# Optimization experiments

Hardware: AMD Instinct MI355X
Metric: run time of the kernel (lower is better)

The kernel has to match this reference:

```python
import jax, jax.numpy as jnp
import numpy as np

K = 7          # kernel_size (square)
P = K // 2     # padding
NUM_HEADS = 12


def setup_inputs() -> dict:
    key = jax.random.key(0)
    ks = jax.random.split(key, 6)
    B, H, W, D = 16, 56, 56, 768
    x = jax.random.normal(ks[0], (B, H, W, D), jnp.float32)
    qkv_w = jax.random.normal(ks[1], (3 * D, D), jnp.float32) * 0.02
    qkv_b = jnp.zeros((3 * D,), jnp.float32)
    rel_bias = jax.random.normal(ks[2], (1, NUM_HEADS, 1, K * K), jnp.float32)
    proj_w = jax.random.normal(ks[3], (D, D), jnp.float32) * 0.02
    proj_b = jnp.zeros((D,), jnp.float32)
    return {"x": x, "qkv_w": qkv_w, "qkv_b": qkv_b, "rel_bias": rel_bias,
            "proj_w": proj_w, "proj_b": proj_b}


def reference(x, qkv_w, qkv_b, rel_bias, proj_w, proj_b):
    B, H, W, D = x.shape
    hd = D // NUM_HEADS
    scale = 1.0 / np.sqrt(hd)

    qkv = x @ qkv_w.T + qkv_b                       # [B,H,W,3D]
    qkv = jnp.pad(qkv, ((0, 0), (P, P), (P, P), (0, 0)))  # zero-pad spatially
    Hp, Wp = H + 2 * P, W + 2 * P
    qkv = qkv.reshape(B, Hp, Wp, 3, NUM_HEADS, hd)
    qkv = jnp.transpose(qkv, (3, 0, 4, 1, 2, 5))    # [3,B,nh,Hp,Wp,hd]
    qf, kf, vf = qkv[0], qkv[1], qkv[2]

    q = qf[:, :, P:P + H, P:P + W, :]               # [B,nh,H,W,hd] (center pixel queries)

    # validity of each padded position (out-of-bounds keys get -inf, matching the torch mask)
    valid = jnp.pad(jnp.ones((H, W), dtype=bool), ((P, P), (P, P)))

    # scores per kernel offset; offsets iterate row-major (di, dj) matching
    # torch.meshgrid(..., indexing='ij') flattening used for relative_position_bias
    scores = []
    for di in range(K):
        for dj in range(K):
            ksh = kf[:, :, di:di + H, dj:dj + W, :]           # shifted keys [B,nh,H,W,hd]
            s = jnp.einsum('bnhwd,bnhwd->bnhw', q, ksh) * scale
            s = s + rel_bias[0, :, 0, di * K + dj][None, :, None, None]
            vmask = valid[di:di + H, dj:dj + W]
            s = jnp.where(vmask[None, None, :, :], s, -jnp.inf)
            scores.append(s)
    scores = jnp.stack(scores, axis=-1)             # [B,nh,H,W,K*K]
    attn = jax.nn.softmax(scores, axis=-1)

    out = jnp.zeros_like(q)
    for di in range(K):
        for dj in range(K):
            vsh = vf[:, :, di:di + H, dj:dj + W, :]
            out = out + attn[..., di * K + dj, None] * vsh

    out = jnp.transpose(out, (0, 2, 3, 1, 4)).reshape(B, H, W, D)
    return out @ proj_w.T + proj_b
```

## Files before the change

### kernel.cpp

```cpp
#include <hip/hip_runtime.h>
#include <hip/hip_bf16.h>

typedef __attribute__((ext_vector_type(8))) short short8;
typedef __attribute__((ext_vector_type(4))) short s16x4;
typedef __attribute__((ext_vector_type(4))) float f32x4;

#define AS1 __attribute__((address_space(1)))
#define AS3 __attribute__((address_space(3)))

__device__ __forceinline__ void gld16(const short* g, short* l) {
  __builtin_amdgcn_global_load_lds((const AS1 void*)g, (AS3 void*)l, 16, 0, 0);
}

__device__ __forceinline__ float bf2f(short x) {
  return __uint_as_float(((unsigned)(unsigned short)x) << 16);
}
__device__ __forceinline__ short f2bf(float f) {
  unsigned u = __float_as_uint(f);
  return (short)((u + 0x7fffu + ((u >> 16) & 1u)) >> 16);
}
__device__ __forceinline__ short f2bfn(float f) {
  __hip_bfloat16 h = __float2bfloat16(f);
  return *reinterpret_cast<short*>(&h);
}

__global__ void cast_f32_bf16(const float* __restrict__ src, short* __restrict__ dst, int n8) {
  int stride = gridDim.x * blockDim.x;
  for (int i = blockIdx.x * blockDim.x + threadIdx.x; i < n8; i += stride) {
    const float4* s = (const float4*)(src + (size_t)i * 8);
    float4 a = s[0], b = s[1];
    short8 o;
    o[0] = f2bf(a.x); o[1] = f2bf(a.y); o[2] = f2bf(a.z); o[3] = f2bf(a.w);
    o[4] = f2bf(b.x); o[5] = f2bf(b.y); o[6] = f2bf(b.z); o[7] = f2bf(b.w);
    *(short8*)(dst + (size_t)i * 8) = o;
  }
}

template<int OUT_BF16>
__global__ __launch_bounds__(256, 2) void gemm_bt(
    const short* __restrict__ A, const short* __restrict__ Bm,
    const float* __restrict__ bias, void* __restrict__ C,
    int M, int N, int Kd, int NB)
{
  __shared__ short As[128 * 64];
  __shared__ short Bs[128 * 64];
  const int tid = threadIdx.x;
  const int wave = tid >> 6, lane = tid & 63;

  int nwg = gridDim.x;
  int chunk = nwg >> 3;
  int bid = blockIdx.x;
  int nb2 = (bid & 7) * chunk + (bid >> 3);
  int per = NB << 3;
  int sr = nb2 / per, rem = nb2 - sr * per;
  int nblk = rem >> 3, mrow = rem & 7;
  int mblk = sr * 8 + mrow;

  size_t arow0 = (size_t)mblk * 128;
  size_t brow0 = (size_t)nblk * 128;
  const int wm = wave >> 1, wn = wave & 1;
  const int lr = lane & 15, grp = lane >> 4;

  const short* gsa[4]; const short* gsb[4];
  short* lda[4]; short* ldb[4];
  #pragma unroll
  for (int i = 0; i < 4; ++i) {
    int f = i * 256 + wave * 64 + lane;
    int row = f >> 3;
    int colc = (f & 7) ^ (row & 7);
    gsa[i] = A  + (arow0 + row) * Kd + colc * 8;
    gsb[i] = Bm + (brow0 + row) * Kd + colc * 8;
    lda[i] = &As[(i * 256 + wave * 64) * 8];
    ldb[i] = &Bs[(i * 256 + wave * 64) * 8];
  }

  f32x4 acc[4][4];
  #pragma unroll
  for (int i = 0; i < 4; ++i)
    #pragma unroll
    for (int j = 0; j < 4; ++j) {
      acc[i][j][0] = 0.f; acc[i][j][1] = 0.f; acc[i][j][2] = 0.f; acc[i][j][3] = 0.f;
    }

  int aoff[4][2], boff[4][2];
  #pragma unroll
  for (int mi = 0; mi < 4; ++mi) {
    int arow = wm * 64 + mi * 16 + lr;
    int brow = wn * 64 + mi * 16 + lr;
    #pragma unroll
    for (int kk = 0; kk < 2; ++kk) {
      int cb = (kk * 64 + grp * 16);
      aoff[mi][kk] = arow * 64 + ((cb ^ ((arow & 7) << 4)) >> 1);
      boff[mi][kk] = brow * 64 + ((cb ^ ((brow & 7) << 4)) >> 1);
    }
  }

  for (int k0 = 0; k0 < Kd; k0 += 64) {
    #pragma unroll
    for (int i = 0; i < 4; ++i) {
      gld16(gsa[i] + k0, lda[i]);
      gld16(gsb[i] + k0, ldb[i]);
    }
    __syncthreads();
    short8 af[4][2], bfr[4][2];
    #pragma unroll
    for (int mi = 0; mi < 4; ++mi)
      #pragma unroll
      for (int kk = 0; kk < 2; ++kk) {
        af[mi][kk]  = *(const short8*)&As[aoff[mi][kk]];
        bfr[mi][kk] = *(const short8*)&Bs[boff[mi][kk]];
      }
    #pragma unroll
    for (int kk = 0; kk < 2; ++kk)
      #pragma unroll
      for (int i = 0; i < 4; ++i)
        #pragma unroll
        for (int j = 0; j < 4; ++j)
          acc[i][j] = __builtin_amdgcn_mfma_f32_16x16x32_bf16(af[i][kk], bfr[j][kk], acc[i][j], 0, 0, 0);
    __syncthreads();
  }

  int r0 = grp * 4;
  #pragma unroll
  for (int i = 0; i < 4; ++i) {
    size_t grow0 = arow0 + wm * 64 + i * 16 + r0;
    #pragma unroll
    for (int j = 0; j < 4; ++j) {
      size_t gcol = brow0 + wn * 64 + j * 16 + lr;
      float bv = bias[gcol];
      #pragma unroll
      for (int r = 0; r < 4; ++r) {
        float v = acc[i][j][r] + bv;
        size_t off = (grow0 + r) * (size_t)N + gcol;
        if (OUT_BF16) ((short*)C)[off] = f2bf(v);
        else          ((float*)C)[off] = v;
      }
    }
  }
}

__global__ void build_idx(unsigned char* __restrict__ idxt) {
  int tile = blockIdx.x;
  int ht = tile >> 2, wt = tile & 3;
  int tid = threadIdx.x;
  int wave = tid >> 6, lane = tid & 63;
  int grp = lane >> 4, q = lane & 15;
  int Sw = (22 * wave) & ~7;
  unsigned w[12];
  #pragma unroll
  for (int i = 0; i < 12; ++i) w[i] = 0x31313131u;
  #pragma unroll
  for (int kt = 0; kt < 10; ++kt) {
    unsigned wd = 0;
    #pragma unroll
    for (int r = 0; r < 4; ++r) {
      int i22 = Sw + kt * 16 + grp * 4 + r;
      int hr = i22 / 22, hc = i22 - hr * 22;
      int dr = hr - wave, dc = hc - q;
      int kh = ht * 4 - 3 + hr, kw = wt * 16 - 3 + hc;
      bool valid = ((unsigned)dr < 7u) && ((unsigned)dc < 7u) &&
                   ((unsigned)kh < 56u) && ((unsigned)kw < 56u);
      unsigned o = valid ? (unsigned)(dr * 7 + dc) : 49u;
      wd |= o << (r * 8);
    }
    w[kt] = wd;
  }
  uint4* dst = (uint4*)(idxt + (((size_t)tile * 4 + wave) * 64 + lane) * 48);
  dst[0] = make_uint4(w[0], w[1], w[2], w[3]);
  dst[1] = make_uint4(w[4], w[5], w[6], w[7]);
  dst[2] = make_uint4(w[8], w[9], w[10], w[11]);
}

#define HALO_V 232

__global__ __launch_bounds__(256, 4) void attn_mfma(
    const short* __restrict__ qkv, const float* __restrict__ rel_bias,
    const unsigned char* __restrict__ idxt, const short* __restrict__ zp,
    short* __restrict__ attn_out)
{
  __shared__ __align__(16) short kvbuf[HALO_V * 64];
  __shared__ float sbias[52];

  const int tid = threadIdx.x;
  const int wave = tid >> 6, lane = tid & 63;
  const int tile = blockIdx.x;
  const int ht = tile >> 2, wt = tile & 3;
  const int head = blockIdx.y % 12, b = blockIdx.y / 12;
  const int r0 = ht * 4, c0 = wt * 16;
  const int grp = lane >> 4, q = lane & 15;
  const int grp4 = grp * 4, grp8 = grp * 8;
  const int Sw = (22 * wave) & ~7;

  if (tid < 50) sbias[tid] = (tid < 49) ? rel_bias[head * 49 + tid] : -1e30f;

  const uint4* ip = (const uint4*)(idxt + (((size_t)tile * 4 + wave) * 64 + lane) * 48);
  uint4 iw0 = ip[0], iw1 = ip[1], iw2 = ip[2];
  unsigned idxw[10] = {iw0.x, iw0.y, iw0.z, iw0.w, iw1.x, iw1.y, iw1.z, iw1.w,
                       iw2.x, iw2.y};

  const int qrow = r0 + wave;
  const int qcol = min(c0 + q, 55);
  const short* qp = qkv + ((size_t)((b * 56 + qrow) * 56 + qcol)) * 2304 + head * 64;
  short8 qf0 = *(const short8*)(qp + grp8);
  short8 qf1 = *(const short8*)(qp + 32 + grp8);

  #pragma unroll
  for (int it = 0; it < 8; ++it) {
    int f = it * 256 + tid;
    if (f < HALO_V * 8) {
      int row = f >> 3, cc = f & 7;
      int hr = row / 22, hc = row - hr * 22;
      int gh = r0 - 3 + hr, gw = c0 - 3 + hc;
      bool ok = (row < 220) && ((unsigned)gh < 56u) && ((unsigned)gw < 56u);
      const short* src = ok
        ? qkv + ((size_t)((b * 56 + gh) * 56 + gw)) * 2304 + 768 + head * 64
              + ((cc ^ (row & 7)) * 8)
        : zp;
      gld16(src, &kvbuf[(it * 256 + wave * 64) * 8]);
    }
  }

  __syncthreads();

  short8 va[4], vb[4];
  int vq = 0, dcc = 0;
  const bool vact = (tid < HALO_V);
  if (vact) {
    vq = tid % 58; dcc = tid / 58;
    #pragma unroll
    for (int rr = 0; rr < 4; ++rr) {
      int vec = vq * 4 + rr;
      int hr = vec / 22, hc = vec - hr * 22;
      int gh = r0 - 3 + hr, gw = c0 - 3 + hc;
      bool ok = (vec < 220) && ((unsigned)gh < 56u) && ((unsigned)gw < 56u);
      const short8* vp = ok
        ? (const short8*)(qkv + ((size_t)((b * 56 + gh) * 56 + gw)) * 2304
                          + 1536 + head * 64 + dcc * 16)
        : (const short8*)zp;
      va[rr] = vp[0]; vb[rr] = vp[1];
    }
  }

  f32x4 accs[10];
  #pragma unroll
  for (int kt = 0; kt < 10; ++kt) {
    accs[kt][0] = 0.f; accs[kt][1] = 0.f; accs[kt][2] = 0.f; accs[kt][3] = 0.f;
  }
  #pragma unroll
  for (int kt = 0; kt < 10; ++kt) {
    int vec = Sw + kt * 16 + q;
    int sw = vec & 7;
    short8 k0 = *(const short8*)&kvbuf[vec * 64 + ((grp ^ sw)) * 8];
    short8 k1 = *(const short8*)&kvbuf[vec * 64 + (((grp + 4) ^ sw)) * 8];
    accs[kt] = __builtin_amdgcn_mfma_f32_16x16x32_bf16(k0, qf0, accs[kt], 0, 0, 0);
    accs[kt] = __builtin_amdgcn_mfma_f32_16x16x32_bf16(k1, qf1, accs[kt], 0, 0, 0);
  }

  __syncthreads();

  float mx = -1e30f;
  #pragma unroll
  for (int kt = 0; kt < 10; ++kt) {
    #pragma unroll
    for (int r = 0; r < 4; ++r) {
      float bia = sbias[(idxw[kt] >> (r * 8)) & 0xffu];
      float s = fmaf(accs[kt][r], 0.125f, bia);
      accs[kt][r] = s;
      mx = fmaxf(mx, s);
    }
  }
  mx = fmaxf(mx, __shfl_xor(mx, 16));
  mx = fmaxf(mx, __shfl_xor(mx, 32));
  float sum = 0.f;
  #pragma unroll
  for (int kt = 0; kt < 10; ++kt)
    #pragma unroll
    for (int r = 0; r < 4; ++r) {
      float e = __expf(accs[kt][r] - mx);
      accs[kt][r] = e;
      sum += e;
    }
  sum += __shfl_xor(sum, 16);
  sum += __shfl_xor(sum, 32);
  float inv = 1.0f / sum;

  if (vact) {
    #pragma unroll
    for (int dd = 0; dd < 8; ++dd) {
      s16x4 w;
      w[0] = va[0][dd]; w[1] = va[1][dd]; w[2] = va[2][dd]; w[3] = va[3][dd];
      *(s16x4*)&kvbuf[(dcc * 16 + dd) * HALO_V + vq * 4] = w;
    }
    #pragma unroll
    for (int dd = 0; dd < 8; ++dd) {
      s16x4 w;
      w[0] = vb[0][dd]; w[1] = vb[1][dd]; w[2] = vb[2][dd]; w[3] = vb[3][dd];
      *(s16x4*)&kvbuf[(dcc * 16 + 8 + dd) * HALO_V + vq * 4] = w;
    }
  }

  unsigned plo[10], phi[10];
  #pragma unroll
  for (int kt = 0; kt < 10; ++kt) {
    plo[kt] = (unsigned)(unsigned short)f2bfn(accs[kt][0])
            | ((unsigned)(unsigned short)f2bfn(accs[kt][1]) << 16);
    phi[kt] = (unsigned)(unsigned short)f2bfn(accs[kt][2])
            | ((unsigned)(unsigned short)f2bfn(accs[kt][3]) << 16);
  }

  __syncthreads();

  const int src0 = ((grp & 1) << 5) + q;
  const bool hi = (grp >> 1) & 1;
  f32x4 acco[4];
  #pragma unroll
  for (int dt = 0; dt < 4; ++dt) {
    acco[dt][0] = 0.f; acco[dt][1] = 0.f; acco[dt][2] = 0.f; acco[dt][3] = 0.f;
  }
  #pragma unroll
  for (int km = 0; km < 5; ++km) {
    int aw0 = __shfl((int)plo[2*km], src0),      bw0 = __shfl((int)plo[2*km+1], src0);
    int aw1 = __shfl((int)phi[2*km], src0),      bw1 = __shfl((int)phi[2*km+1], src0);
    int aw2 = __shfl((int)plo[2*km], src0 + 16), bw2 = __shfl((int)plo[2*km+1], src0 + 16);
    int aw3 = __shfl((int)phi[2*km], src0 + 16), bw3 = __shfl((int)phi[2*km+1], src0 + 16);
    int4 wv = make_int4(hi ? bw0 : aw0, hi ? bw1 : aw1,
                        hi ? bw2 : aw2, hi ? bw3 : aw3);
    short8 pf = *(short8*)&wv;
    #pragma unroll
    for (int dt = 0; dt < 4; ++dt) {
      short8 vf = *(const short8*)&kvbuf[(dt * 16 + q) * HALO_V + Sw + km * 32 + grp8];
      acco[dt] = __builtin_amdgcn_mfma_f32_16x16x32_bf16(pf, vf, acco[dt], 0, 0, 0);
    }
  }

  float invr[4];
  #pragma unroll
  for (int r = 0; r < 4; ++r) invr[r] = __shfl(inv, grp4 + r);
  #pragma unroll
  for (int dt = 0; dt < 4; ++dt) {
    #pragma unroll
    for (int r = 0; r < 4; ++r) {
      int qc = c0 + grp4 + r;
      if (qc < 56) {
        size_t off = ((size_t)((b * 56 + qrow) * 56 + qc)) * 768
                     + head * 64 + dt * 16 + q;
        attn_out[off] = f2bfn(acco[dt][r] * invr[r]);
      }
    }
  }
}

extern "C" void kernel_launch(void* const* d_in, const int* in_sizes, int n_in,
                              void* d_out, int out_size, void* d_ws, size_t ws_size,
                              hipStream_t stream)
{
  const float* x      = (const float*)d_in[0];
  const float* qkv_w  = (const float*)d_in[1];
  const float* qkv_b  = (const float*)d_in[2];
  const float* rel_b  = (const float*)d_in[3];
  const float* proj_w = (const float*)d_in[4];
  const float* proj_b = (const float*)d_in[5];

  char* ws = (char*)d_ws;
  short* x_bf    = (short*)(ws);
  short* attn_bf = (short*)(ws);
  short* qw_bf   = (short*)(ws + 77070336);
  short* pw_bf   = (short*)(ws + 80609280);
  short* qkv_bf  = (short*)(ws + 81788928);
  unsigned char* idxt = (unsigned char*)(ws + 312999936);
  short* zp      = (short*)(ws + 313688064);

  hipMemsetAsync(zp, 0, 256, stream);
  build_idx<<<56, 256, 0, stream>>>(idxt);

  cast_f32_bf16<<<2048, 256, 0, stream>>>(x, x_bf, 38535168 / 8);
  cast_f32_bf16<<<864, 256, 0, stream>>>(qkv_w, qw_bf, 1769472 / 8);
  cast_f32_bf16<<<288, 256, 0, stream>>>(proj_w, pw_bf, 589824 / 8);

  gemm_bt<1><<<392 * 18, 256, 0, stream>>>(x_bf, qw_bf, qkv_b, (void*)qkv_bf,
                                           50176, 2304, 768, 18);

  attn_mfma<<<dim3(56, 192), 256, 0, stream>>>(qkv_bf, rel_b, idxt, zp, attn_bf);

  gemm_bt<0><<<392 * 6, 256, 0, stream>>>(attn_bf, pw_bf, proj_b, d_out,
                                          50176, 768, 768, 6);
}
```

Measured before the change: 461.3 us.

## Use 256x256 double-buffered GEMM tiles with 512 threads and prefetch overlap

Replaces the 128x128 single-buffered bf16 GEMM with a 256x256 tile kernel run by 8 waves. Shared-memory loads are double-buffered so the next K-slice is fetched while MFMAs run, with explicit vmcnt waits, raw barriers and s_setprio around the MFMA blocks. The XCD-aware block remap is generalised to grid sizes not divisible by 8. The larger tile raises per-block reuse, but it uses 128KB of LDS and many accumulator registers, which can cut occupancy. The proj GEMM also drops to only 588 blocks, which may leave some compute units underused.

```diff
diff --git a/kernel.cpp b/kernel.cpp
--- a/kernel.cpp
+++ b/kernel.cpp
@@ -37,93 +37,123 @@
 }
 
 template<int OUT_BF16>
-__global__ __launch_bounds__(256, 2) void gemm_bt(
+__global__ __launch_bounds__(512, 2) void gemm256(
     const short* __restrict__ A, const short* __restrict__ Bm,
     const float* __restrict__ bias, void* __restrict__ C,
     int M, int N, int Kd, int NB)
 {
-  __shared__ short As[128 * 64];
-  __shared__ short Bs[128 * 64];
+  __shared__ short As[2][256 * 64];
+  __shared__ short Bs[2][256 * 64];
   const int tid = threadIdx.x;
   const int wave = tid >> 6, lane = tid & 63;
 
   int nwg = gridDim.x;
-  int chunk = nwg >> 3;
-  int bid = blockIdx.x;
-  int nb2 = (bid & 7) * chunk + (bid >> 3);
-  int per = NB << 3;
+  int q8 = nwg >> 3, r8 = nwg & 7;
+  int xcd = blockIdx.x & 7, loc = blockIdx.x >> 3;
+  int nb2 = (xcd < r8 ? xcd * (q8 + 1) : r8 * (q8 + 1) + (xcd - r8) * q8) + loc;
+  int per = NB << 2;
   int sr = nb2 / per, rem = nb2 - sr * per;
-  int nblk = rem >> 3, mrow = rem & 7;
-  int mblk = sr * 8 + mrow;
-
-  size_t arow0 = (size_t)mblk * 128;
-  size_t brow0 = (size_t)nblk * 128;
-  const int wm = wave >> 1, wn = wave & 1;
+  int nblk = rem >> 2, mrow = rem & 3;
+  int mblk = sr * 4 + mrow;
+
+  size_t arow0 = (size_t)mblk * 256;
+  size_t brow0 = (size_t)nblk * 256;
+  const int wm = wave >> 2, wn = wave & 3;
   const int lr = lane & 15, grp = lane >> 4;
 
-  const short* gsa[4]; const short* gsb[4];
-  short* lda[4]; short* ldb[4];
+  const short* gsa[4]; const short* gsb[4]; int sdst[4];
   #pragma unroll
   for (int i = 0; i < 4; ++i) {
-    int f = i * 256 + wave * 64 + lane;
+    int f = i * 512 + tid;
     int row = f >> 3;
     int colc = (f & 7) ^ (row & 7);
     gsa[i] = A  + (arow0 + row) * Kd + colc * 8;
     gsb[i] = Bm + (brow0 + row) * Kd + colc * 8;
-    lda[i] = &As[(i * 256 + wave * 64) * 8];
-    ldb[i] = &Bs[(i * 256 + wave * 64) * 8];
-  }
-
-  f32x4 acc[4][4];
-  #pragma unroll
-  for (int i = 0; i < 4; ++i)
+    sdst[i] = (i * 512 + wave * 64) * 8;
+  }
+
+  f32x4 acc[8][4];
+  #pragma unroll
+  for (int i = 0; i < 8; ++i)
     #pragma unroll
     for (int j = 0; j < 4; ++j) {
       acc[i][j][0] = 0.f; acc[i][j][1] = 0.f; acc[i][j][2] = 0.f; acc[i][j][3] = 0.f;
     }
 
-  int aoff[4][2], boff[4][2];
-  #pragma unroll
-  for (int mi = 0; mi < 4; ++mi) {
-    int arow = wm * 64 + mi * 16 + lr;
-    int brow = wn * 64 + mi * 16 + lr;
+  int aoff[8][2], boff[4][2];
+  #pragma unroll
+  for (int mi = 0; mi < 8; ++mi) {
+    int arow = wm * 128 + mi * 16 + lr;
     #pragma unroll
     for (int kk = 0; kk < 2; ++kk) {
-      int cb = (kk * 64 + grp * 16);
+      int cb = kk * 64 + grp * 16;
       aoff[mi][kk] = arow * 64 + ((cb ^ ((arow & 7) << 4)) >> 1);
-      boff[mi][kk] = brow * 64 + ((cb ^ ((brow & 7) << 4)) >> 1);
-    }
-  }
-
-  for (int k0 = 0; k0 < Kd; k0 += 64) {
-    #pragma unroll
-    for (int i = 0; i < 4; ++i) {
-      gld16(gsa[i] + k0, lda[i]);
-      gld16(gsb[i] + k0, ldb[i]);
-    }
-    __syncthreads();
-    short8 af[4][2], bfr[4][2];
-    #pragma unroll
-    for (int mi = 0; mi < 4; ++mi)
+    }
+  }
+  #pragma unroll
+  for (int nj = 0; nj < 4; ++nj) {
+    int brow = wn * 64 + nj * 16 + lr;
+    #pragma unroll
+    for (int kk = 0; kk < 2; ++kk) {
+      int cb = kk * 64 + grp * 16;
+      boff[nj][kk] = brow * 64 + ((cb ^ ((brow & 7) << 4)) >> 1);
+    }
+  }
+
+  const int NK = Kd >> 6;
+
+  #pragma unroll
+  for (int i = 0; i < 4; ++i) gld16(gsa[i], &As[0][sdst[i]]);
+  #pragma unroll
+  for (int i = 0; i < 4; ++i) gld16(gsb[i], &Bs[0][sdst[i]]);
+
+  int cur = 0;
+  for (int t = 0; t < NK; ++t) {
+    if (t + 1 < NK) {
+      int koff = (t + 1) << 6;
       #pragma unroll
-      for (int kk = 0; kk < 2; ++kk) {
-        af[mi][kk]  = *(const short8*)&As[aoff[mi][kk]];
-        bfr[mi][kk] = *(const short8*)&Bs[boff[mi][kk]];
+      for (int i = 0; i < 4; ++i) gld16(gsa[i] + koff, &As[cur ^ 1][sdst[i]]);
+      #pragma unroll
+      for (int i = 0; i < 4; ++i) gld16(gsb[i] + koff, &Bs[cur ^ 1][sdst[i]]);
+      asm volatile("s_waitcnt vmcnt(8)" ::: "memory");
+    } else {
+      asm volatile("s_waitcnt vmcnt(0)" ::: "memory");
+    }
+    __builtin_amdgcn_s_barrier();
+    asm volatile("" ::: "memory");
+
+    const short* pa = As[cur];
+    const short* pb = Bs[cur];
+    #pragma unroll
+    for (int kk = 0; kk < 2; ++kk) {
+      short8 bfr[4];
+      #pragma unroll
+      for (int nj = 0; nj < 4; ++nj) bfr[nj] = *(const short8*)&pb[boff[nj][kk]];
+      #pragma unroll
+      for (int mh = 0; mh < 2; ++mh) {
+        short8 af[4];
+        #pragma unroll
+        for (int r = 0; r < 4; ++r) af[r] = *(const short8*)&pa[aoff[mh * 4 + r][kk]];
+        __builtin_amdgcn_s_setprio(1);
+        #pragma unroll
+        for (int r = 0; r < 4; ++r)
+          #pragma unroll
+          for (int nj = 0; nj < 4; ++nj)
+            acc[mh * 4 + r][nj] = __builtin_amdgcn_mfma_f32_16x16x32_bf16(
+                af[r], bfr[nj], acc[mh * 4 + r][nj], 0, 0, 0);
+        __builtin_amdgcn_s_setprio(0);
       }
-    #pragma unroll
-    for (int kk = 0; kk < 2; ++kk)
-      #pragma unroll
-      for (int i = 0; i < 4; ++i)
-        #pragma unroll
-        for (int j = 0; j < 4; ++j)
-          acc[i][j] = __builtin_amdgcn_mfma_f32_16x16x32_bf16(af[i][kk], bfr[j][kk], acc[i][j], 0, 0, 0);
-    __syncthreads();
+    }
+    asm volatile("" ::: "memory");
+    __builtin_amdgcn_s_barrier();
+    asm volatile("" ::: "memory");
+    cur ^= 1;
   }
 
   int r0 = grp * 4;
   #pragma unroll
-  for (int i = 0; i < 4; ++i) {
-    size_t grow0 = arow0 + wm * 64 + i * 16 + r0;
+  for (int i = 0; i < 8; ++i) {
+    size_t grow0 = arow0 + wm * 128 + i * 16 + r0;
     #pragma unroll
     for (int j = 0; j < 4; ++j) {
       size_t gcol = brow0 + wn * 64 + j * 16 + lr;
@@ -377,11 +407,11 @@
   cast_f32_bf16<<<864, 256, 0, stream>>>(qkv_w, qw_bf, 1769472 / 8);
   cast_f32_bf16<<<288, 256, 0, stream>>>(proj_w, pw_bf, 589824 / 8);
 
-  gemm_bt<1><<<392 * 18, 256, 0, stream>>>(x_bf, qw_bf, qkv_b, (void*)qkv_bf,
-                                           50176, 2304, 768, 18);
+  gemm256<1><<<1764, 512, 0, stream>>>(x_bf, qw_bf, qkv_b, (void*)qkv_bf,
+                                       50176, 2304, 768, 9);
 
   attn_mfma<<<dim3(56, 192), 256, 0, stream>>>(qkv_bf, rel_b, idxt, zp, attn_bf);
 
-  gemm_bt<0><<<392 * 6, 256, 0, stream>>>(attn_bf, pw_bf, proj_b, d_out,
-                                          50176, 768, 768, 6);
-}
+  gemm256<0><<<588, 512, 0, stream>>>(attn_bf, pw_bf, proj_b, d_out,
+                                      50176, 768, 768, 3);
+}
```

After: 483.6 us. 1.05x slower.
